# Optimization experiments

Hardware: AMD Instinct MI355X
Metric: run time of the kernel (lower is better)

## Reference

```python
import jax, jax.numpy as jnp
import numpy as np

N_NODES = 100000


def gcn_conv(x, src, dst, dinv, W, b):
    # PyG GCNConv: h = D^-1/2 (A+I) D^-1/2 (x W) + b
    h = x @ W                                   # [N, out]
    norm = dinv[src] * dinv[dst]                # [E'] edge weights
    msg = norm[:, None] * h[src]                # gather + scale
    agg = jax.ops.segment_sum(msg, dst, num_segments=x.shape[0])
    return agg + b


def setup_inputs() -> dict:
    key = jax.random.key(0)
    ks = jax.random.split(key, 8)
    x = jax.random.normal(ks[0], (N_NODES, 64), dtype=jnp.float32)
    edge_index = jax.random.randint(ks[1], (2, 1600000), 0, N_NODES, dtype=jnp.int32)
    s = 0.1
    return {
        "x": x,
        "edge_index": edge_index,
        "W1": jax.random.normal(ks[2], (64, 64), dtype=jnp.float32) * s,
        "b1": jnp.zeros((64,), dtype=jnp.float32),
        "W2": jax.random.normal(ks[3], (64, 32), dtype=jnp.float32) * s,
        "b2": jnp.zeros((32,), dtype=jnp.float32),
        "W3": jax.random.normal(ks[4], (32, 2), dtype=jnp.float32) * s,
        "b3": jnp.zeros((2,), dtype=jnp.float32),
    }


def reference(x, edge_index, W1, b1, W2, b2, W3, b3):
    n = x.shape[0]
    loop = jnp.arange(n, dtype=edge_index.dtype)
    src = jnp.concatenate([edge_index[0], loop])  # add self-loops
    dst = jnp.concatenate([edge_index[1], loop])
    deg = jax.ops.segment_sum(jnp.ones_like(dst, dtype=x.dtype), dst, num_segments=n)
    dinv = jnp.where(deg > 0, jax.lax.rsqrt(jnp.maximum(deg, 1.0)), 0.0)
    h = jax.nn.relu(gcn_conv(x, src, dst, dinv, W1, b1))
    h = jax.nn.relu(gcn_conv(h, src, dst, dinv, W2, b2))
    return gcn_conv(h, src, dst, dinv, W3, b3)
```

## Files before the change

kernel.cpp:

```cpp
#include <hip/hip_runtime.h>
#include <hip/hip_fp16.h>

#define N_NODES 100000
#define N_EDGES 1600000
#define BSHIFT 9
#define NBUCK ((N_NODES + 511) / 512)
#define BCAP 12288

__global__ void bucket1_kernel(const int* __restrict__ src, const int* __restrict__ dst,
                               int* __restrict__ gbcount, int* __restrict__ bbuf, int E) {
    __shared__ int hcnt[NBUCK];
    __shared__ int hbase[NBUCK];
    int t = threadIdx.x;
    for (int i = t; i < NBUCK; i += 256) hcnt[i] = 0;
    __syncthreads();
    int e0 = blockIdx.x * 2048 + t;
    int ss[8], dd[8];
#pragma unroll
    for (int u = 0; u < 8; u++) {
        int e = e0 + u * 256;
        if (e < E) {
            ss[u] = src[e];
            dd[u] = dst[e];
            atomicAdd(&hcnt[dd[u] >> BSHIFT], 1);
        } else {
            dd[u] = -1;
        }
    }
    __syncthreads();
    for (int i = t; i < NBUCK; i += 256) {
        int c = hcnt[i];
        hbase[i] = c ? atomicAdd(&gbcount[i], c) : 0;
        hcnt[i] = 0;
    }
    __syncthreads();
#pragma unroll
    for (int u = 0; u < 8; u++) {
        if (dd[u] >= 0) {
            int bk = dd[u] >> BSHIFT;
            int r = atomicAdd(&hcnt[bk], 1);
            bbuf[(size_t)bk * BCAP + hbase[bk] + r] = ss[u] | ((dd[u] & 511) << 17);
        }
    }
}

__global__ void scan196_kernel(const int* __restrict__ gbcount, int* __restrict__ gbase,
                               int* __restrict__ rowptrN, int E) {
    __shared__ int s[256];
    int t = threadIdx.x;
    int v = (t < NBUCK) ? gbcount[t] : 0;
    s[t] = v;
    __syncthreads();
    for (int off = 1; off < 256; off <<= 1) {
        int u = (t >= off) ? s[t - off] : 0;
        __syncthreads();
        s[t] += u;
        __syncthreads();
    }
    if (t < NBUCK) gbase[t] = s[t] - v;
    if (t == 0) *rowptrN = E;
}

__global__ __launch_bounds__(512)
void bucket2_kernel(const int* __restrict__ bbuf, const int* __restrict__ gbcount,
                    const int* __restrict__ gbase, int* __restrict__ rowptr,
                    float* __restrict__ dinv, int* __restrict__ eidx, int N) {
    int b = blockIdx.x;
    int base_node = b << BSHIFT;
    int nn = min(512, N - base_node);
    int t = threadIdx.x;
    __shared__ int s[512];
    __shared__ int cur[512];
    s[t] = 0;
    __syncthreads();
    int sz = gbcount[b];
    const int* eb = bbuf + (size_t)b * BCAP;
    for (int j = t; j < sz; j += 512) atomicAdd(&s[((unsigned)eb[j]) >> 17], 1);
    __syncthreads();
    int myc = s[t];
    if (t < nn) dinv[base_node + t] = rsqrtf((float)myc + 1.0f);
    __syncthreads();
    for (int off = 1; off < 512; off <<= 1) {
        int u = (t >= off) ? s[t - off] : 0;
        __syncthreads();
        s[t] += u;
        __syncthreads();
    }
    int rp = gbase[b] + s[t] - myc;
    if (t < nn) rowptr[base_node + t] = rp;
    cur[t] = rp;
    __syncthreads();
    for (int j = t; j < sz; j += 512) {
        int e = eb[j];
        int pos = atomicAdd(&cur[((unsigned)e) >> 17], 1);
        eidx[pos] = e & 0x1FFFF;
    }
}

__global__ void sortrow_wave(const int* __restrict__ rowptr, int* __restrict__ eidx, int n) {
    int g = (blockIdx.x * blockDim.x + threadIdx.x) >> 6;
    int lane = threadIdx.x & 63;
    if (g >= n) return;
    int start = rowptr[g];
    int end = rowptr[g + 1];
    int len = end - start;
    if (len <= 1) return;

    if (len <= 64) {
        int v = (lane < len) ? eidx[start + lane] : 0x7fffffff;
#pragma unroll
        for (int k = 2; k <= 64; k <<= 1) {
#pragma unroll
            for (int j = k >> 1; j > 0; j >>= 1) {
                int partner = __shfl_xor(v, j, 64);
                bool up = ((lane & k) == 0);
                bool keepMin = (((lane & j) == 0) == up);
                int mn = min(v, partner), mx = max(v, partner);
                v = keepMin ? mn : mx;
            }
        }
        if (lane < len) eidx[start + lane] = v;
    } else if (lane == 0) {
        for (int i = start + 1; i < end; i++) {
            int key = eidx[i];
            int j = i - 1;
            while (j >= start && eidx[j] > key) { eidx[j + 1] = eidx[j]; j--; }
            eidx[j + 1] = key;
        }
    }
}

template <int FIN, int FOUT>
__global__ __launch_bounds__(256, 2)
void gemm_tiled(const float* __restrict__ in, const float* __restrict__ W,
                const float* __restrict__ dinv, __half* __restrict__ out, int n) {
    constexpr int CG = FOUT / 4;
    constexpr int RG = 256 / CG;
    constexpr int TR = RG * 4;
    constexpr int LDA = FIN + 4;
    __shared__ float sIn[TR * LDA];
    __shared__ float sW[FIN * FOUT];

    for (int i = threadIdx.x; i < FIN * FOUT / 4; i += 256)
        ((float4*)sW)[i] = ((const float4*)W)[i];

    int r0 = blockIdx.x * TR;
    for (int i = threadIdx.x; i < TR * FIN / 4; i += 256) {
        int rr = i / (FIN / 4);
        int cc = i % (FIN / 4);
        int gr = r0 + rr;
        float4 v = (gr < n) ? ((const float4*)in)[(size_t)gr * (FIN / 4) + cc]
                            : make_float4(0.f, 0.f, 0.f, 0.f);
        *(float4*)&sIn[rr * LDA + cc * 4] = v;
    }
    __syncthreads();

    int tc = threadIdx.x % CG;
    int tr = threadIdx.x / CG;
    int rbase = tr * 4, cbase = tc * 4;
    float acc[4][4] = {};

#pragma unroll 2
    for (int k = 0; k < FIN; k += 4) {
        float4 a[4], b[4];
#pragma unroll
        for (int i = 0; i < 4; i++) a[i] = *(float4*)&sIn[(rbase + i) * LDA + k];
#pragma unroll
        for (int kk = 0; kk < 4; kk++) b[kk] = *(float4*)&sW[(k + kk) * FOUT + cbase];
#pragma unroll
        for (int i = 0; i < 4; i++) {
            acc[i][0] += a[i].x * b[0].x + a[i].y * b[1].x + a[i].z * b[2].x + a[i].w * b[3].x;
            acc[i][1] += a[i].x * b[0].y + a[i].y * b[1].y + a[i].z * b[2].y + a[i].w * b[3].y;
            acc[i][2] += a[i].x * b[0].z + a[i].y * b[1].z + a[i].z * b[2].z + a[i].w * b[3].z;
            acc[i][3] += a[i].x * b[0].w + a[i].y * b[1].w + a[i].z * b[2].w + a[i].w * b[3].w;
        }
    }

#pragma unroll
    for (int i = 0; i < 4; i++) {
        int gr = r0 + rbase + i;
        if (gr < n) {
            float dv = dinv[gr];
            union { __half h[4]; uint2 u; } pk;
            pk.h[0] = __float2half_rn(dv * acc[i][0]);
            pk.h[1] = __float2half_rn(dv * acc[i][1]);
            pk.h[2] = __float2half_rn(dv * acc[i][2]);
            pk.h[3] = __float2half_rn(dv * acc[i][3]);
            *(uint2*)&out[(size_t)gr * FOUT + cbase] = pk.u;
        }
    }
}

template <int FIN, int FOUT, bool OUT_HALF>
__global__ __launch_bounds__(256, 4)
void agg_gemm_kernel(const int* __restrict__ eidx, const int* __restrict__ rowptr,
                     const float* __restrict__ dinv, const __half* __restrict__ h,
                     const float* __restrict__ bias, const float* __restrict__ W,
                     void* __restrict__ outv, int n) {
    constexpr int L = 8;
    constexpr int PH = FIN / L;
    constexpr int NODES = 256 / L;
    constexpr int SVS = FIN + 1;
    using vh = _Float16 __attribute__((ext_vector_type(PH)));
    __shared__ float sW[FIN * FOUT];
    __shared__ float sv[NODES * SVS];

    for (int i = threadIdx.x; i < FIN * FOUT / 4; i += 256)
        ((float4*)sW)[i] = ((const float4*)W)[i];

    int g = (blockIdx.x * blockDim.x + threadIdx.x) / L;
    int lane = threadIdx.x % L;
    int slot = threadIdx.x / L;
    float di = 0.f;

    if (g < n) {
        int j = rowptr[g];
        int end = rowptr[g + 1];
        di = dinv[g];
        const __half* hb = h + lane * PH;

        float acc0[PH], acc1[PH];
#pragma unroll
        for (int q = 0; q < PH; q++) { acc0[q] = 0.f; acc1[q] = 0.f; }

        for (; j + 8 <= end; j += 8) {
            int s0 = eidx[j];
            int s1 = eidx[j + 1];
            int s2 = eidx[j + 2];
            int s3 = eidx[j + 3];
            int s4 = eidx[j + 4];
            int s5 = eidx[j + 5];
            int s6 = eidx[j + 6];
            int s7 = eidx[j + 7];
            vh v0 = *(const vh*)(hb + (size_t)s0 * FIN);
            vh v1 = *(const vh*)(hb + (size_t)s1 * FIN);
            vh v2 = *(const vh*)(hb + (size_t)s2 * FIN);
            vh v3 = *(const vh*)(hb + (size_t)s3 * FIN);
            vh v4 = *(const vh*)(hb + (size_t)s4 * FIN);
            vh v5 = *(const vh*)(hb + (size_t)s5 * FIN);
            vh v6 = *(const vh*)(hb + (size_t)s6 * FIN);
            vh v7 = *(const vh*)(hb + (size_t)s7 * FIN);
#pragma unroll
            for (int q = 0; q < PH; q++) {
                acc0[q] += (float)v0[q] + (float)v2[q];
                acc1[q] += (float)v1[q] + (float)v3[q];
                acc0[q] += (float)v4[q] + (float)v6[q];
                acc1[q] += (float)v5[q] + (float)v7[q];
            }
        }
        for (; j + 2 <= end; j += 2) {
            int s0 = eidx[j];
            int s1 = eidx[j + 1];
            vh v0 = *(const vh*)(hb + (size_t)s0 * FIN);
            vh v1 = *(const vh*)(hb + (size_t)s1 * FIN);
#pragma unroll
            for (int q = 0; q < PH; q++) { acc0[q] += (float)v0[q]; acc1[q] += (float)v1[q]; }
        }
        if (j < end) {
            vh v = *(const vh*)(hb + (size_t)eidx[j] * FIN);
#pragma unroll
            for (int q = 0; q < PH; q++) acc0[q] += (float)v[q];
        }

        vh sf = *(const vh*)(hb + (size_t)g * FIN);
        float* svn = &sv[slot * SVS + lane * PH];
#pragma unroll
        for (int q = 0; q < PH; q++) {
            float v = di * ((acc0[q] + acc1[q]) + (float)sf[q]) + bias[lane * PH + q];
            svn[q] = fmaxf(v, 0.f);
        }
    }
    __syncthreads();

    if (g < n) {
        const float* vn = &sv[slot * SVS];
        if constexpr (OUT_HALF) {
            constexpr int PC = FOUT / L;
            float o[PC] = {};
            for (int k = 0; k < FIN; k++) {
                float vk = vn[k];
                float4 w = *(const float4*)&sW[k * FOUT + lane * PC];
                o[0] += vk * w.x; o[1] += vk * w.y; o[2] += vk * w.z; o[3] += vk * w.w;
            }
            union { __half h[4]; uint2 u; } pk;
#pragma unroll
            for (int q = 0; q < PC; q++) pk.h[q] = __float2half_rn(di * o[q]);
            *(uint2*)((__half*)outv + (size_t)g * FOUT + lane * PC) = pk.u;
        } else {
            if (lane < FOUT) {
                float o = 0.f;
                for (int k = 0; k < FIN; k++) o += vn[k] * sW[k * FOUT + lane];
                ((float*)outv)[(size_t)g * FOUT + lane] = di * o;
            }
        }
    }
}

template <int F>
__global__ void agg_kernel(const int* __restrict__ eidx, const int* __restrict__ rowptr,
                           const float* __restrict__ dinv, const float* __restrict__ h,
                           const float* __restrict__ b, float* __restrict__ out, int n) {
    int g = (blockIdx.x * blockDim.x + threadIdx.x) / F;
    int lane = threadIdx.x % F;
    if (g >= n) return;
    int j = rowptr[g];
    int end = rowptr[g + 1];
    float di = dinv[g];
    float hs = h[(size_t)g * F + lane];

    float acc0 = 0.f, acc1 = 0.f, acc2 = 0.f, acc3 = 0.f;
    float acc4 = 0.f, acc5 = 0.f, acc6 = 0.f, acc7 = 0.f;
    for (; j + 8 <= end; j += 8) {
        int s0 = eidx[j];
        int s1 = eidx[j + 1];
        int s2 = eidx[j + 2];
        int s3 = eidx[j + 3];
        int s4 = eidx[j + 4];
        int s5 = eidx[j + 5];
        int s6 = eidx[j + 6];
        int s7 = eidx[j + 7];
        acc0 += h[(size_t)s0 * F + lane];
        acc1 += h[(size_t)s1 * F + lane];
        acc2 += h[(size_t)s2 * F + lane];
        acc3 += h[(size_t)s3 * F + lane];
        acc4 += h[(size_t)s4 * F + lane];
        acc5 += h[(size_t)s5 * F + lane];
        acc6 += h[(size_t)s6 * F + lane];
        acc7 += h[(size_t)s7 * F + lane];
    }
    for (; j + 2 <= end; j += 2) {
        int s0 = eidx[j];
        int s1 = eidx[j + 1];
        acc0 += h[(size_t)s0 * F + lane];
        acc1 += h[(size_t)s1 * F + lane];
    }
    if (j < end) {
        acc2 += h[(size_t)eidx[j] * F + lane];
    }
    float acc = ((acc0 + acc1) + (acc2 + acc3)) + ((acc4 + acc5) + (acc6 + acc7));
    out[(size_t)g * F + lane] = di * (acc + hs) + b[lane];
}

extern "C" void kernel_launch(void* const* d_in, const int* in_sizes, int n_in,
                              void* d_out, int out_size, void* d_ws, size_t ws_size,
                              hipStream_t stream) {
    const float* x  = (const float*)d_in[0];
    const int* ei   = (const int*)d_in[1];
    const float* W1 = (const float*)d_in[2];
    const float* b1 = (const float*)d_in[3];
    const float* W2 = (const float*)d_in[4];
    const float* b2 = (const float*)d_in[5];
    const float* W3 = (const float*)d_in[6];
    const float* b3 = (const float*)d_in[7];
    float* out = (float*)d_out;

    const int N = N_NODES;
    const int E = N_EDGES;
    const int* src = ei;
    const int* dst = ei + E;

    char* p = (char*)d_ws;
    int*    rowptr  = (int*)p;            p += ((size_t)(N + 1) * 4 + 15) / 16 * 16;
    float*  dinv    = (float*)p;          p += ((size_t)N * 4 + 15) / 16 * 16;
    int*    gbcount = (int*)p;            p += ((size_t)NBUCK * 4 + 15) / 16 * 16;
    int*    gbase   = (int*)p;            p += ((size_t)NBUCK * 4 + 15) / 16 * 16;
    int*    eidx    = (int*)p;            p += (size_t)E * 4;
    __half* A1      = (__half*)p;         p += (size_t)N * 64 * 2;
    __half* A2      = (__half*)p;         p += (size_t)N * 32 * 2;
    float*  A3      = (float*)p;          p += (size_t)N * 2 * 4;
    int*    bbuf    = (int*)p;

    const int T = 256;

    hipMemsetAsync(gbcount, 0, NBUCK * sizeof(int), stream);
    bucket1_kernel<<<(E + 2047) / 2048, T, 0, stream>>>(src, dst, gbcount, bbuf, E);
    scan196_kernel<<<1, 256, 0, stream>>>(gbcount, gbase, rowptr + N, E);
    bucket2_kernel<<<NBUCK, 512, 0, stream>>>(bbuf, gbcount, gbase, rowptr, dinv, eidx, N);
    sortrow_wave<<<(N * 64 + T - 1) / T, T, 0, stream>>>(rowptr, eidx, N);

    gemm_tiled<64, 64><<<(N + 63) / 64, T, 0, stream>>>(x, W1, dinv, A1, N);

    agg_gemm_kernel<64, 32, true><<<(N + 31) / 32, T, 0, stream>>>(
        eidx, rowptr, dinv, A1, b1, W2, A2, N);

    agg_gemm_kernel<32, 2, false><<<(N + 31) / 32, T, 0, stream>>>(
        eidx, rowptr, dinv, A2, b2, W3, A3, N);

    agg_kernel<2><<<(N * 2 + T - 1) / T, T, 0, stream>>>(eidx, rowptr, dinv, A3, b3, out, N);
}
```

Before: 268.0 us.

## Process nodes in degree-sorted order to balance aggregation work across waves

Builds a degree histogram during CSR construction, scans it in descending order, and scatters node ids into a permutation grouped by in-degree. The aggregation kernels then take their node from this permutation, so nodes of similar degree share a wavefront and lanes idle less on divergent loop trip counts. This adds two small kernels and an indirection, and output writes become scattered rather than contiguous. Nodes sharing a degree are placed in nondeterministic order, which may reduce memory locality.

Result: slower. 288.7 us (+7.7%).

```diff
diff --git a/kernel.cpp b/kernel.cpp
--- a/kernel.cpp
+++ b/kernel.cpp
@@ -64,21 +64,27 @@
 __global__ __launch_bounds__(512)
 void bucket2_kernel(const int* __restrict__ bbuf, const int* __restrict__ gbcount,
                     const int* __restrict__ gbase, int* __restrict__ rowptr,
-                    float* __restrict__ dinv, int* __restrict__ eidx, int N) {
+                    float* __restrict__ dinv, int* __restrict__ eidx,
+                    int* __restrict__ dhist, int N) {
     int b = blockIdx.x;
     int base_node = b << BSHIFT;
     int nn = min(512, N - base_node);
     int t = threadIdx.x;
     __shared__ int s[512];
     __shared__ int cur[512];
+    __shared__ int dh[64];
     s[t] = 0;
+    if (t < 64) dh[t] = 0;
     __syncthreads();
     int sz = gbcount[b];
     const int* eb = bbuf + (size_t)b * BCAP;
     for (int j = t; j < sz; j += 512) atomicAdd(&s[((unsigned)eb[j]) >> 17], 1);
     __syncthreads();
     int myc = s[t];
-    if (t < nn) dinv[base_node + t] = rsqrtf((float)myc + 1.0f);
+    if (t < nn) {
+        dinv[base_node + t] = rsqrtf((float)myc + 1.0f);
+        atomicAdd(&dh[min(myc, 63)], 1);
+    }
     __syncthreads();
     for (int off = 1; off < 512; off <<= 1) {
         int u = (t >= off) ? s[t - off] : 0;
@@ -90,11 +96,47 @@
     if (t < nn) rowptr[base_node + t] = rp;
     cur[t] = rp;
     __syncthreads();
+    if (t < 64) {
+        int c = dh[t];
+        if (c) atomicAdd(&dhist[t], c);
+    }
     for (int j = t; j < sz; j += 512) {
         int e = eb[j];
         int pos = atomicAdd(&cur[((unsigned)e) >> 17], 1);
         eidx[pos] = e & 0x1FFFF;
     }
+}
+
+__global__ void scan64_kernel(const int* __restrict__ dhist, int* __restrict__ dcur) {
+    int t = threadIdx.x;
+    int v = dhist[63 - t];
+    int x = v;
+#pragma unroll
+    for (int off = 1; off < 64; off <<= 1) {
+        int u = __shfl_up(x, off, 64);
+        if (t >= off) x += u;
+    }
+    dcur[63 - t] = x - v;
+}
+
+__global__ void perm_scatter(const int* __restrict__ rowptr, int* __restrict__ dcur,
+                             int* __restrict__ perm, int n) {
+    __shared__ int lh[64];
+    __shared__ int lbase[64];
+    int t = threadIdx.x;
+    int g = blockIdx.x * 256 + t;
+    if (t < 64) lh[t] = 0;
+    __syncthreads();
+    int r = 0, bin = 0;
+    if (g < n) {
+        int deg = rowptr[g + 1] - rowptr[g];
+        bin = min(deg, 63);
+        r = atomicAdd(&lh[bin], 1);
+    }
+    __syncthreads();
+    if (t < 64) lbase[t] = lh[t] ? atomicAdd(&dcur[t], lh[t]) : 0;
+    __syncthreads();
+    if (g < n) perm[lbase[bin] + r] = g;
 }
 
 __global__ void sortrow_wave(const int* __restrict__ rowptr, int* __restrict__ eidx, int n) {
@@ -193,7 +235,8 @@
 
 template <int FIN, int FOUT, bool OUT_HALF>
 __global__ __launch_bounds__(256, 4)
-void agg_gemm_kernel(const int* __restrict__ eidx, const int* __restrict__ rowptr,
+void agg_gemm_kernel(const int* __restrict__ perm, const int* __restrict__ eidx,
+                     const int* __restrict__ rowptr,
                      const float* __restrict__ dinv, const __half* __restrict__ h,
                      const float* __restrict__ bias, const float* __restrict__ W,
                      void* __restrict__ outv, int n) {
@@ -208,7 +251,8 @@
     for (int i = threadIdx.x; i < FIN * FOUT / 4; i += 256)
         ((float4*)sW)[i] = ((const float4*)W)[i];
 
-    int g = (blockIdx.x * blockDim.x + threadIdx.x) / L;
+    int gg = (blockIdx.x * blockDim.x + threadIdx.x) / L;
+    int g = (gg < n) ? perm[gg] : n;
     int lane = threadIdx.x % L;
     int slot = threadIdx.x / L;
     float di = 0.f;
@@ -297,12 +341,14 @@
 }
 
 template <int F>
-__global__ void agg_kernel(const int* __restrict__ eidx, const int* __restrict__ rowptr,
+__global__ void agg_kernel(const int* __restrict__ perm, const int* __restrict__ eidx,
+                           const int* __restrict__ rowptr,
                            const float* __restrict__ dinv, const float* __restrict__ h,
                            const float* __restrict__ b, float* __restrict__ out, int n) {
-    int g = (blockIdx.x * blockDim.x + threadIdx.x) / F;
+    int gg = (blockIdx.x * blockDim.x + threadIdx.x) / F;
     int lane = threadIdx.x % F;
-    if (g >= n) return;
+    if (gg >= n) return;
+    int g = perm[gg];
     int j = rowptr[g];
     int end = rowptr[g + 1];
     float di = dinv[g];
@@ -362,8 +408,11 @@
     char* p = (char*)d_ws;
     int*    rowptr  = (int*)p;            p += ((size_t)(N + 1) * 4 + 15) / 16 * 16;
     float*  dinv    = (float*)p;          p += ((size_t)N * 4 + 15) / 16 * 16;
-    int*    gbcount = (int*)p;            p += ((size_t)NBUCK * 4 + 15) / 16 * 16;
+    int*    gbcount = (int*)p;            p += (size_t)NBUCK * 4;
+    int*    dhist   = (int*)p;            p += 64 * 4;
     int*    gbase   = (int*)p;            p += ((size_t)NBUCK * 4 + 15) / 16 * 16;
+    int*    dcur    = (int*)p;            p += 64 * 4;
+    int*    perm    = (int*)p;            p += (size_t)N * 4;
     int*    eidx    = (int*)p;            p += (size_t)E * 4;
     __half* A1      = (__half*)p;         p += (size_t)N * 64 * 2;
     __half* A2      = (__half*)p;         p += (size_t)N * 32 * 2;
@@ -372,19 +421,22 @@
 
     const int T = 256;
 
-    hipMemsetAsync(gbcount, 0, NBUCK * sizeof(int), stream);
+    hipMemsetAsync(gbcount, 0, (NBUCK + 64) * sizeof(int), stream);
     bucket1_kernel<<<(E + 2047) / 2048, T, 0, stream>>>(src, dst, gbcount, bbuf, E);
     scan196_kernel<<<1, 256, 0, stream>>>(gbcount, gbase, rowptr + N, E);
-    bucket2_kernel<<<NBUCK, 512, 0, stream>>>(bbuf, gbcount, gbase, rowptr, dinv, eidx, N);
+    bucket2_kernel<<<NBUCK, 512, 0, stream>>>(bbuf, gbcount, gbase, rowptr, dinv, eidx,
+                                              dhist, N);
+    scan64_kernel<<<1, 64, 0, stream>>>(dhist, dcur);
+    perm_scatter<<<(N + 255) / 256, T, 0, stream>>>(rowptr, dcur, perm, N);
     sortrow_wave<<<(N * 64 + T - 1) / T, T, 0, stream>>>(rowptr, eidx, N);
 
     gemm_tiled<64, 64><<<(N + 63) / 64, T, 0, stream>>>(x, W1, dinv, A1, N);
 
     agg_gemm_kernel<64, 32, true><<<(N + 31) / 32, T, 0, stream>>>(
-        eidx, rowptr, dinv, A1, b1, W2, A2, N);
+        perm, eidx, rowptr, dinv, A1, b1, W2, A2, N);
 
     agg_gemm_kernel<32, 2, false><<<(N + 31) / 32, T, 0, stream>>>(
-        eidx, rowptr, dinv, A2, b2, W3, A3, N);
-
-    agg_kernel<2><<<(N * 2 + T - 1) / T, T, 0, stream>>>(eidx, rowptr, dinv, A3, b3, out, N);
-}
+        perm, eidx, rowptr, dinv, A2, b2, W3, A3, N);
+
+    agg_kernel<2><<<(N * 2 + T - 1) / T, T, 0, stream>>>(perm, eidx, rowptr, dinv, A3, b3, out, N);
+}
```
